# Kernel tuning notes

Hardware: AMD Instinct MI355X
Metric: run time of the kernel (lower is better)

The kernel has to match this reference:

```python
import jax, jax.numpy as jnp
import numpy as np

EPS = 1e-8

def unit_projection(x):
    # project each embedding vector so its Fourier coefficients have unit magnitude
    f = jnp.fft.fft(x, axis=-1)
    f = f / jnp.maximum(jnp.abs(f), EPS)
    return jnp.real(jnp.fft.ifft(f, axis=-1))

def bind(a, b):
    return jnp.fft.irfft(jnp.fft.rfft(a, axis=-1) * jnp.fft.rfft(b, axis=-1), n=a.shape[-1], axis=-1)

def unbind(s, k):
    # k is unit-magnitude in Fourier domain, so its inverse is its conjugate
    return jnp.fft.irfft(jnp.fft.rfft(s, axis=-1) * jnp.conj(jnp.fft.rfft(k, axis=-1)), n=s.shape[-1], axis=-1)

def layer_norm(x, g, b):
    mu = jnp.mean(x, axis=-1, keepdims=True)
    var = jnp.var(x, axis=-1, keepdims=True)
    return (x - mu) * jax.lax.rsqrt(var + 1e-5) * g + b

def setup_inputs():
    key = jax.random.key(0)
    ks = jax.random.split(key, 12)
    B, S, D = 4, 2048, 1024
    sc = 1.0 / np.sqrt(D)
    inp = {
        'x': jax.random.normal(ks[0], (B, S, D), jnp.float32),
        'Wq': jax.random.normal(ks[1], (D, D), jnp.float32) * sc,
        'bq': jnp.zeros((D,), jnp.float32),
        'Wk': jax.random.normal(ks[2], (D, D), jnp.float32) * sc,
        'bk': jnp.zeros((D,), jnp.float32),
        'Wv': jax.random.normal(ks[3], (D, D), jnp.float32) * sc,
        'bv': jnp.zeros((D,), jnp.float32),
        'ln1_g': jnp.ones((D,), jnp.float32), 'ln1_b': jnp.zeros((D,), jnp.float32),
        'ln2_g': jnp.ones((D,), jnp.float32), 'ln2_b': jnp.zeros((D,), jnp.float32),
        'W1': jax.random.normal(ks[4], (D, 4 * D), jnp.float32) * sc,
        'b1': jnp.zeros((4 * D,), jnp.float32),
        'W2': jax.random.normal(ks[5], (4 * D, D), jnp.float32) * (1.0 / np.sqrt(4 * D)),
        'b2': jnp.zeros((D,), jnp.float32),
    }
    return inp

def reference(x, Wq, bq, Wk, bk, Wv, bv, ln1_g, ln1_b, ln2_g, ln2_b, W1, b1, W2, b2):
    h = layer_norm(x, ln1_g, ln1_b)
    q = unit_projection(h @ Wq + bq)
    k = unit_projection(h @ Wk + bk)
    v = unit_projection(h @ Wv + bv)
    s = jnp.cumsum(bind(k, v), axis=1)  # causal prefix-sum over sequence
    mixed = unbind(s, q)
    x = x + mixed  # dropout=0.0
    h2 = layer_norm(x, ln2_g, ln2_b)
    mlp = jax.nn.gelu(h2 @ W1 + b1, approximate=False) @ W2 + b2
    return x + mlp
```

## Files before the change

### kernel.cpp

```cpp
#include <hip/hip_runtime.h>
#include <cstdint>
#include <cstddef>

#define DD 1024
#define SSEQ 2048
#define NB 4
#define MROWS 8192
#define FBINS 513
#define FPAD 520
#define WFP 1152
#define NQKV 3456
#define NHID 4096
#define NCHUNK 64
#define SCHUNK 32

typedef _Float16 f16_t;
typedef _Float16 f16x8 __attribute__((ext_vector_type(8)));
typedef _Float16 f16x2 __attribute__((ext_vector_type(2)));
typedef float f32x4 __attribute__((ext_vector_type(4)));

__device__ __forceinline__ float2 cmul(float2 a, float2 b) {
  return make_float2(a.x * b.x - a.y * b.y, a.x * b.y + a.y * b.x);
}

__device__ __forceinline__ void async_cp16(const void* g, void* l) {
  __builtin_amdgcn_global_load_lds(
      (const __attribute__((address_space(1))) void*)g,
      (__attribute__((address_space(3))) void*)l, 16, 0, 0);
}

__device__ __forceinline__ float fast_gelu(float val) {
  float av = __builtin_fabsf(val);
  float z = av * 0.70710678118654752f;
  float t = __builtin_amdgcn_rcpf(__builtin_fmaf(0.3275911f, z, 1.0f));
  float poly = t * __builtin_fmaf(t,
      __builtin_fmaf(t, __builtin_fmaf(t,
          __builtin_fmaf(t, 1.061405429f, -1.453152027f),
          1.421413741f), -0.284496736f), 0.254829592f);
  float e = __builtin_amdgcn_exp2f(z * z * -1.4426950408889634f);
  float w = poly * e;
  float r = fmaxf(val, 0.0f);
  return __builtin_fmaf(-0.5f * av, w, r);
}

__device__ __forceinline__ void fft1024(float2* bufA, float2* bufB,
                                        const float2* tw, int tid) {
  float2* s = bufA;
  float2* d = bufB;
  for (int m = 1; m < 1024; m <<= 1) {
#pragma unroll
    for (int r2 = 0; r2 < 2; ++r2) {
      int u = tid + r2 * 256;
      int k = u & (m - 1);
      int jm = u - k;
      float2 c0 = s[u];
      float2 c1 = s[u + 512];
      float2 wt = tw[jm];
      float2 su = make_float2(c0.x + c1.x, c0.y + c1.y);
      float2 df = make_float2(c0.x - c1.x, c0.y - c1.y);
      float2 pr = cmul(wt, df);
      d[2 * jm + k] = su;
      d[2 * jm + k + m] = pr;
    }
    __syncthreads();
    float2* tmp = s; s = d; d = tmp;
  }
}

__device__ __forceinline__ float2* fft512(float2* bufA, float2* bufB,
                                          const float2* tw, int tid) {
  float2* s = bufA;
  float2* d = bufB;
  for (int m = 1; m < 512; m <<= 1) {
    int u = tid;
    int k = u & (m - 1);
    int jm = u - k;
    float2 c0 = s[u];
    float2 c1 = s[u + 256];
    float2 wt = tw[jm];
    float2 su = make_float2(c0.x + c1.x, c0.y + c1.y);
    float2 df = make_float2(c0.x - c1.x, c0.y - c1.y);
    float2 pr = cmul(wt, df);
    d[2 * jm + k] = su;
    d[2 * jm + k + m] = pr;
    __syncthreads();
    float2* tmp = s; s = d; d = tmp;
  }
  return s;
}

__global__ __launch_bounds__(256) void wfft_k(
    const float* __restrict__ Wq, const float* __restrict__ Wk,
    const float* __restrict__ Wv, float* __restrict__ WfAll) {
  __shared__ float2 tw[512];
  __shared__ float2 bufA[1024];
  __shared__ float2 bufB[1024];
  const int tid = threadIdx.x;
  const int p = blockIdx.x >> 10, k = blockIdx.x & 1023;
  const float* W = (p == 0) ? Wq : ((p == 1) ? Wk : Wv);
  for (int t = tid; t < 512; t += 256) {
    float ang = -6.2831853071795864769f * (float)t * (1.0f / 1024.0f);
    tw[t] = make_float2(cosf(ang), sinf(ang));
  }
  const float* src = W + (size_t)k * DD;
  for (int t = tid; t < 1024; t += 256) bufA[t] = make_float2(src[t], 0.f);
  __syncthreads();
  fft1024(bufA, bufB, tw, tid);
  float* dst = WfAll + ((size_t)p * DD + k) * WFP;
  for (int t = tid; t <= 512; t += 256) {
    float2 f = bufA[t];
    dst[2 * t] = f.x;
    dst[2 * t + 1] = f.y;
  }
  for (int j = 1026 + tid; j < WFP; j += 256) dst[j] = 0.f;
}

__global__ __launch_bounds__(256) void bfft_k(
    const float* __restrict__ bq, const float* __restrict__ bk,
    const float* __restrict__ bv, float* __restrict__ biasC) {
  __shared__ float2 tw[512];
  __shared__ float2 bufA[1024];
  __shared__ float2 bufB[1024];
  const int tid = threadIdx.x;
  const int p = blockIdx.x;
  const float* bsrc = (p == 0) ? bq : ((p == 1) ? bk : bv);
  for (int t = tid; t < 512; t += 256) {
    float ang = -6.2831853071795864769f * (float)t * (1.0f / 1024.0f);
    tw[t] = make_float2(cosf(ang), sinf(ang));
  }
  for (int t = tid; t < 1024; t += 256) bufA[t] = make_float2(bsrc[t], 0.f);
  __syncthreads();
  fft1024(bufA, bufB, tw, tid);
  float* dst = biasC + (size_t)p * WFP;
  for (int t = tid; t <= 512; t += 256) {
    float2 f = bufA[t];
    dst[2 * t] = f.x;
    dst[2 * t + 1] = f.y;
  }
  for (int j = 1026 + tid; j < WFP; j += 256) dst[j] = 0.f;
}

__global__ __launch_bounds__(256) void transpose_cast_k(
    const float* __restrict__ W, f16_t* __restrict__ Wt, int K, int N) {
  __shared__ float tile[32][33];
  const int tx = threadIdx.x & 31, ty = threadIdx.x >> 5;
  const int n0 = blockIdx.x * 32, k0 = blockIdx.y * 32;
#pragma unroll
  for (int i = 0; i < 32; i += 8)
    tile[ty + i][tx] = W[(size_t)(k0 + ty + i) * N + n0 + tx];
  __syncthreads();
#pragma unroll
  for (int i = 0; i < 32; i += 8)
    Wt[(size_t)(n0 + ty + i) * K + k0 + tx] = (f16_t)tile[tx][ty + i];
}

__global__ __launch_bounds__(256) void transpose_cast2_k(
    const float* __restrict__ W, f16_t* __restrict__ WtH,
    f16_t* __restrict__ WtL, int K, int N) {
  __shared__ float tile[32][33];
  const int tx = threadIdx.x & 31, ty = threadIdx.x >> 5;
  const int n0 = blockIdx.x * 32, k0 = blockIdx.y * 32;
#pragma unroll
  for (int i = 0; i < 32; i += 8)
    tile[ty + i][tx] = W[(size_t)(k0 + ty + i) * N + n0 + tx];
  __syncthreads();
#pragma unroll
  for (int i = 0; i < 32; i += 8) {
    float val = tile[tx][ty + i];
    f16_t hi = (f16_t)val;
    f16_t lo = (f16_t)(val - (float)hi);
    size_t idx = (size_t)(n0 + ty + i) * K + k0 + tx;
    WtH[idx] = hi;
    WtL[idx] = lo;
  }
}

__global__ __launch_bounds__(256) void ln_cast2_k(
    const float* __restrict__ x, const float* __restrict__ g,
    const float* __restrict__ b, f16_t* __restrict__ hH,
    f16_t* __restrict__ hL) {
  const int row = blockIdx.x, tid = threadIdx.x;
  __shared__ float red[8];
  const float* xr = x + (size_t)row * DD;
  float v[4], ls = 0.f, lq = 0.f;
#pragma unroll
  for (int i = 0; i < 4; ++i) {
    v[i] = xr[i * 256 + tid];
    ls += v[i];
    lq += v[i] * v[i];
  }
#pragma unroll
  for (int o = 32; o > 0; o >>= 1) {
    ls += __shfl_down(ls, o);
    lq += __shfl_down(lq, o);
  }
  const int lane = tid & 63, w = tid >> 6;
  if (lane == 0) { red[w] = ls; red[w + 4] = lq; }
  __syncthreads();
  const float S = red[0] + red[1] + red[2] + red[3];
  const float Q = red[4] + red[5] + red[6] + red[7];
  const float mean = S * (1.f / 1024.f);
  const float var = Q * (1.f / 1024.f) - mean * mean;
  const float rs = rsqrtf(var + 1e-5f);
#pragma unroll
  for (int i = 0; i < 4; ++i) {
    int n = i * 256 + tid;
    float val = (v[i] - mean) * rs * g[n] + b[n];
    f16_t hi = (f16_t)val;
    hH[(size_t)row * DD + n] = hi;
    hL[(size_t)row * DD + n] = (f16_t)(val - (float)hi);
  }
}

__global__ __launch_bounds__(256, 2) void gemm_qkv_k(
    const f16_t* __restrict__ Ahi, const f16_t* __restrict__ Alo,
    const f16_t* __restrict__ Bhi, const float* __restrict__ bias,
    float* __restrict__ outF) {
  __shared__ alignas(16) f16_t AsH[128 * 64];
  __shared__ alignas(16) f16_t AsL[128 * 64];
  __shared__ alignas(16) f16_t BsH[128 * 64];
  const int tid = threadIdx.x;
  const int lane = tid & 63;
  const int w = tid >> 6;
  const int wm = w >> 1, wn = w & 1;

  const int lin = blockIdx.x;
  const int s = (lin & 7) * 216 + (lin >> 3);
  const int g = s / 108;
  const int r = s % 108;
  const int n = r >> 2;
  const int m0 = g * 4 + (r & 3);
  const int bn = n * 128;
  const int bm = m0 * 128;
  const bool qmode = (n < 9);

  f32x4 acc[4][4];
#pragma unroll
  for (int i = 0; i < 4; ++i)
#pragma unroll
    for (int j = 0; j < 4; ++j) acc[i][j] = (f32x4){0.f, 0.f, 0.f, 0.f};

  const int srow = lane >> 3;
  const int slot = lane & 7;

  for (int kt = 0; kt < 1024; kt += 64) {
#pragma unroll
    for (int i = 0; i < 4; ++i) {
      const int rb = (i * 4 + w) * 8;
      const int row = rb + srow;
      const int gg = (slot - (row & 7)) & 7;
      size_t ga = (size_t)(bm + row) * 1024 + kt + gg * 8;
      size_t gb = (size_t)(bn + row) * 1024 + kt + gg * 8;
      async_cp16(Ahi + ga, &AsH[rb * 64]);
      if (qmode) async_cp16(Alo + ga, &AsL[rb * 64]);
      async_cp16(Bhi + gb, &BsH[rb * 64]);
    }
    __syncthreads();
#pragma unroll
    for (int ks = 0; ks < 2; ++ks) {
      const int cgbase = ks * 4 + (lane >> 4);
      f16x8 ah[4], bh[4];
#pragma unroll
      for (int mt = 0; mt < 4; ++mt) {
        int m = wm * 64 + mt * 16 + (lane & 15);
        int sl = (cgbase + (m & 7)) & 7;
        ah[mt] = *(const f16x8*)(&AsH[m * 64 + sl * 8]);
      }
#pragma unroll
      for (int nt = 0; nt < 4; ++nt) {
        int nn = wn * 64 + nt * 16 + (lane & 15);
        int sl = (cgbase + (nn & 7)) & 7;
        bh[nt] = *(const f16x8*)(&BsH[nn * 64 + sl * 8]);
      }
#pragma unroll
      for (int mt = 0; mt < 4; ++mt)
#pragma unroll
        for (int nt = 0; nt < 4; ++nt)
          acc[mt][nt] = __builtin_amdgcn_mfma_f32_16x16x32_f16(
              ah[mt], bh[nt], acc[mt][nt], 0, 0, 0);
      if (qmode) {
        f16x8 al[4];
#pragma unroll
        for (int mt = 0; mt < 4; ++mt) {
          int m = wm * 64 + mt * 16 + (lane & 15);
          int sl = (cgbase + (m & 7)) & 7;
          al[mt] = *(const f16x8*)(&AsL[m * 64 + sl * 8]);
        }
#pragma unroll
        for (int mt = 0; mt < 4; ++mt)
#pragma unroll
          for (int nt = 0; nt < 4; ++nt)
            acc[mt][nt] = __builtin_amdgcn_mfma_f32_16x16x32_f16(
                al[mt], bh[nt], acc[mt][nt], 0, 0, 0);
      }
    }
    __syncthreads();
  }

  const int q = lane >> 4;
  const int cn = lane & 15;
#pragma unroll
  for (int mt = 0; mt < 4; ++mt) {
#pragma unroll
    for (int nt = 0; nt < 4; ++nt) {
      const int gcol = bn + wn * 64 + nt * 16 + cn;
      const float bv = bias[gcol];
      const int grow0 = bm + wm * 64 + mt * 16 + q * 4;
#pragma unroll
      for (int i = 0; i < 4; ++i) {
        size_t idx = (size_t)(grow0 + i) * NQKV + gcol;
        outF[idx] = acc[mt][nt][i] + bv;
      }
    }
  }
}

template <int EPI>
__global__ __launch_bounds__(256, 2) void gemm_bt_k(
    const f16_t* __restrict__ A, const f16_t* __restrict__ Bt,
    const float* __restrict__ bias, const float* __restrict__ resid,
    float* __restrict__ outF, f16_t* __restrict__ outH, int M, int N, int K) {
  __shared__ alignas(16) f16_t As[128 * 64];
  __shared__ alignas(16) f16_t Bs[128 * 64];
  const int tid = threadIdx.x;
  const int lane = tid & 63;
  const int w = tid >> 6;
  const int wm = w >> 1, wn = w & 1;
  int bm, bn;
  if (EPI == 2) {
    const int ntn = N >> 7;
    const int per = ((N >> 7) * (M >> 7)) >> 3;
    const int s = ((int)blockIdx.x & 7) * per + ((int)blockIdx.x >> 3);
    const int half = ntn * 2;
    const int g = s / half;
    const int r = s % half;
    bn = (r >> 1) * 128;
    bm = (g * 2 + (r & 1)) * 128;
  } else {
    bm = blockIdx.y * 128;
    bn = blockIdx.x * 128;
  }

  f32x4 acc[4][4];
#pragma unroll
  for (int i = 0; i < 4; ++i)
#pragma unroll
    for (int j = 0; j < 4; ++j) acc[i][j] = (f32x4){0.f, 0.f, 0.f, 0.f};

  const int srow = lane >> 3;
  const int slot = lane & 7;

  for (int kt = 0; kt < K; kt += 64) {
#pragma unroll
    for (int i = 0; i < 4; ++i) {
      const int rb = (i * 4 + w) * 8;
      const int row = rb + srow;
      const int gg = (slot - (row & 7)) & 7;
      const f16_t* ga = A + (size_t)(bm + row) * K + kt + gg * 8;
      const f16_t* gb = Bt + (size_t)(bn + row) * K + kt + gg * 8;
      async_cp16(ga, &As[rb * 64]);
      async_cp16(gb, &Bs[rb * 64]);
    }
    __syncthreads();
#pragma unroll
    for (int ks = 0; ks < 2; ++ks) {
      const int cgbase = ks * 4 + (lane >> 4);
      f16x8 af[4], bfv[4];
#pragma unroll
      for (int mt = 0; mt < 4; ++mt) {
        int m = wm * 64 + mt * 16 + (lane & 15);
        int sl = (cgbase + (m & 7)) & 7;
        af[mt] = *(const f16x8*)(&As[m * 64 + sl * 8]);
      }
#pragma unroll
      for (int nt = 0; nt < 4; ++nt) {
        int nn = wn * 64 + nt * 16 + (lane & 15);
        int sl = (cgbase + (nn & 7)) & 7;
        bfv[nt] = *(const f16x8*)(&Bs[nn * 64 + sl * 8]);
      }
#pragma unroll
      for (int mt = 0; mt < 4; ++mt)
#pragma unroll
        for (int nt = 0; nt < 4; ++nt)
          acc[mt][nt] = __builtin_amdgcn_mfma_f32_16x16x32_f16(
              af[mt], bfv[nt], acc[mt][nt], 0, 0, 0);
    }
    __syncthreads();
  }

  const int q = lane >> 4;
  const int cn = lane & 15;
#pragma unroll
  for (int mt = 0; mt < 4; ++mt) {
#pragma unroll
    for (int nt = 0; nt < 4; ++nt) {
      const int gcol = bn + wn * 64 + nt * 16 + cn;
      const float bv = bias[gcol];
      const int grow0 = bm + wm * 64 + mt * 16 + q * 4;
#pragma unroll
      for (int i = 0; i < 4; ++i) {
        float val = acc[mt][nt][i] + bv;
        size_t idx = (size_t)(grow0 + i) * N + gcol;
        if (EPI == 1) {
          outH[idx] = (f16_t)fast_gelu(val);
        } else {
          outF[idx] = val + resid[idx];
        }
      }
    }
  }
}

__device__ __forceinline__ float2 unitc(float2 a) {
  float inv = 1.0f / fmaxf(sqrtf(a.x * a.x + a.y * a.y), 1e-8f);
  return make_float2(a.x * inv, a.y * inv);
}
__device__ __forceinline__ float2 bind_bin(const float2* r, int f) {
  float2 kn = unitc(r[576 + f]);
  float2 vn = unitc(r[1152 + f]);
  return cmul(kn, vn);
}

__global__ __launch_bounds__(256) void scan_pass1_k(
    const float* __restrict__ qkvF, float2* __restrict__ T) {
  const int bid = blockIdx.x;
  const int sc = bid & 63;
  const int fh = (bid >> 6) & 1;
  const int b = bid >> 7;
  const int s0 = sc * SCHUNK;
  const float2* base = (const float2*)(qkvF + ((size_t)(b * SSEQ + s0)) * NQKV);
  for (int f = fh * 256 + threadIdx.x; f < FBINS; f += 512) {
    float2 acc = make_float2(0.f, 0.f);
    const float2* r = base;
    for (int i = 0; i < SCHUNK; ++i) {
      float2 pv = bind_bin(r, f);
      acc.x += pv.x; acc.y += pv.y;
      r += NQKV / 2;
    }
    T[((size_t)b * NCHUNK + sc) * FBINS + f] = acc;
  }
}

__global__ void scan_pass2_k(float2* __restrict__ T) {
  const int idx = blockIdx.x * 256 + threadIdx.x;
  if (idx >= NB * FBINS) return;
  const int b = idx / FBINS, f = idx % FBINS;
  float2 acc = make_float2(0.f, 0.f);
  for (int sc = 0; sc < NCHUNK; ++sc) {
    size_t a = ((size_t)b * NCHUNK + sc) * FBINS + f;
    float2 v = T[a];
    T[a] = acc;
    acc.x += v.x; acc.y += v.y;
  }
}

__global__ __launch_bounds__(256) void scan_pass3_k(
    const float* __restrict__ qkvF, const float2* __restrict__ T,
    float2* __restrict__ Scum) {
  const int bid = blockIdx.x;
  const int sc = bid & 63;
  const int fh = (bid >> 6) & 1;
  const int b = bid >> 7;
  const int s0 = sc * SCHUNK;
  const float2* base = (const float2*)(qkvF + ((size_t)(b * SSEQ + s0)) * NQKV);
  for (int f = fh * 256 + threadIdx.x; f < FBINS; f += 512) {
    float2 acc = T[((size_t)b * NCHUNK + sc) * FBINS + f];
    const float2* r = base;
    size_t orow = ((size_t)(b * SSEQ + s0)) * FPAD + f;
    for (int i = 0; i < SCHUNK; ++i) {
      float2 pv = bind_bin(r, f);
      acc.x += pv.x; acc.y += pv.y;
      Scum[orow] = acc;
      r += NQKV / 2;
      orow += FPAD;
    }
  }
}

__global__ __launch_bounds__(256) void unbind_ln2_k(
    const float2* __restrict__ Scum, const float* __restrict__ qkvF,
    const float* __restrict__ x, float* __restrict__ x2out,
    f16_t* __restrict__ h2, const float* __restrict__ g2,
    const float* __restrict__ b2) {
  __shared__ float2 tw[256];
  __shared__ float2 Marr[513];
  __shared__ float2 bufA[512];
  __shared__ float2 bufB[512];
  __shared__ float red[8];
  const int tid = threadIdx.x;
  const int row = blockIdx.x;

  {
    float ang = 6.2831853071795864769f * (float)tid * (1.0f / 512.0f);
    tw[tid] = make_float2(cosf(ang), sinf(ang));
  }
  const float2* qrow = (const float2*)(qkvF + (size_t)row * NQKV);
  for (int t = tid; t <= 512; t += 256) {
    float2 sc = Scum[(size_t)row * FPAD + t];
    float2 fq = unitc(qrow[t]);
    Marr[t] = make_float2(sc.x * fq.x + sc.y * fq.y, sc.y * fq.x - sc.x * fq.y);
  }
  __syncthreads();
#pragma unroll
  for (int rr = 0; rr < 2; ++rr) {
    int t = tid + rr * 256;
    float2 a = Marr[t];
    float2 b = Marr[512 - t];
    float2 E = make_float2(0.5f * (a.x + b.x), 0.5f * (a.y - b.y));
    float2 Dd = make_float2(0.5f * (a.x - b.x), 0.5f * (a.y + b.y));
    float ang = 6.2831853071795864769f * (float)t * (1.0f / 1024.0f);
    float cw = cosf(ang), sw = sinf(ang);
    float2 O = make_float2(cw * Dd.x - sw * Dd.y, cw * Dd.y + sw * Dd.x);
    bufA[t] = make_float2(E.x - O.y, E.y + O.x);
  }
  __syncthreads();
  float2* res = fft512(bufA, bufB, tw, tid);

  const float* xr = x + (size_t)row * DD;
  float v[2][2];
  float ls = 0.f, lq = 0.f;
#pragma unroll
  for (int rr = 0; rr < 2; ++rr) {
    int n = tid + rr * 256;
    float2 z = res[n];
    float2 xv = *(const float2*)(xr + 2 * n);
    float v0 = xv.x + z.x * (1.0f / 512.0f);
    float v1 = xv.y + z.y * (1.0f / 512.0f);
    *(float2*)(x2out + (size_t)row * DD + 2 * n) = make_float2(v0, v1);
    v[rr][0] = v0; v[rr][1] = v1;
    ls += v0 + v1;
    lq += v0 * v0 + v1 * v1;
  }
#pragma unroll
  for (int o = 32; o > 0; o >>= 1) {
    ls += __shfl_down(ls, o);
    lq += __shfl_down(lq, o);
  }
  const int lane = tid & 63, w = tid >> 6;
  if (lane == 0) { red[w] = ls; red[w + 4] = lq; }
  __syncthreads();
  const float S = red[0] + red[1] + red[2] + red[3];
  const float Q = red[4] + red[5] + red[6] + red[7];
  const float mean = S * (1.f / 1024.f);
  const float var = Q * (1.f / 1024.f) - mean * mean;
  const float rs = rsqrtf(var + 1e-5f);
  f16_t* hr = h2 + (size_t)row * DD;
#pragma unroll
  for (int rr = 0; rr < 2; ++rr) {
    int n = tid + rr * 256;
    float2 gv = *(const float2*)(g2 + 2 * n);
    float2 bv = *(const float2*)(b2 + 2 * n);
    f16x2 hp;
    hp[0] = (f16_t)((v[rr][0] - mean) * rs * gv.x + bv.x);
    hp[1] = (f16_t)((v[rr][1] - mean) * rs * gv.y + bv.y);
    *(f16x2*)(hr + 2 * n) = hp;
  }
}

extern "C" void kernel_launch(void* const* d_in, const int* in_sizes, int n_in,
                              void* d_out, int out_size, void* d_ws,
                              size_t ws_size, hipStream_t stream) {
  const float* x     = (const float*)d_in[0];
  const float* Wq    = (const float*)d_in[1];
  const float* bq    = (const float*)d_in[2];
  const float* Wk    = (const float*)d_in[3];
  const float* bk    = (const float*)d_in[4];
  const float* Wv    = (const float*)d_in[5];
  const float* bv    = (const float*)d_in[6];
  const float* ln1_g = (const float*)d_in[7];
  const float* ln1_b = (const float*)d_in[8];
  const float* ln2_g = (const float*)d_in[9];
  const float* ln2_b = (const float*)d_in[10];
  const float* W1    = (const float*)d_in[11];
  const float* b1    = (const float*)d_in[12];
  const float* W2    = (const float*)d_in[13];
  const float* b2    = (const float*)d_in[14];
  float* out = (float*)d_out;

  char* p = (char*)d_ws;
  auto take = [&](size_t bytes) {
    char* r = p;
    p += (bytes + 255) & ~(size_t)255;
    return r;
  };
  f16_t* BtH   = (f16_t*)take((size_t)NQKV * DD * sizeof(f16_t));
  f16_t* BtL   = (f16_t*)take((size_t)NQKV * DD * sizeof(f16_t));
  f16_t* W1T   = (f16_t*)take((size_t)NHID * DD * sizeof(f16_t));
  f16_t* W2T   = (f16_t*)take((size_t)DD * NHID * sizeof(f16_t));
  float* biasC = (float*)take((size_t)NQKV * sizeof(float));
  f16_t* hbuf  = (f16_t*)take((size_t)MROWS * DD * sizeof(f16_t));
  char*  big   = take((size_t)MROWS * NQKV * sizeof(float));
  float2* Scum = (float2*)take((size_t)MROWS * FPAD * sizeof(float2));
  float* x2    = (float*)take((size_t)MROWS * DD * sizeof(float));
  float2* Tch  = (float2*)take((size_t)NB * NCHUNK * FBINS * sizeof(float2));
  float* WfAll   = (float*)big;
  float* qkv_f   = (float*)big;
  f16_t* mlp1    = (f16_t*)big;
  f16_t* hlo     = (f16_t*)x2;

  wfft_k<<<3 * DD, 256, 0, stream>>>(Wq, Wk, Wv, WfAll);
  for (int pp = 0; pp < 3; ++pp)
    transpose_cast2_k<<<dim3(WFP / 32, DD / 32), 256, 0, stream>>>(
        WfAll + (size_t)pp * DD * WFP,
        BtH + (size_t)pp * WFP * DD,
        BtL + (size_t)pp * WFP * DD, DD, WFP);
  bfft_k<<<3, 256, 0, stream>>>(bq, bk, bv, biasC);
  transpose_cast_k<<<dim3(128, 32), 256, 0, stream>>>(W1, W1T, DD, NHID);
  transpose_cast_k<<<dim3(32, 128), 256, 0, stream>>>(W2, W2T, NHID, DD);

  ln_cast2_k<<<MROWS, 256, 0, stream>>>(x, ln1_g, ln1_b, hbuf, hlo);

  gemm_qkv_k<<<(NQKV / 128) * (MROWS / 128), 256, 0, stream>>>(
      hbuf, hlo, BtH, biasC, qkv_f);

  scan_pass1_k<<<NB * NCHUNK * 2, 256, 0, stream>>>(qkv_f, Tch);
  scan_pass2_k<<<(NB * FBINS + 255) / 256, 256, 0, stream>>>(Tch);
  scan_pass3_k<<<NB * NCHUNK * 2, 256, 0, stream>>>(qkv_f, Tch, Scum);

  unbind_ln2_k<<<MROWS, 256, 0, stream>>>(Scum, qkv_f, x, x2, hbuf, ln2_g, ln2_b);

  gemm_bt_k<1><<<dim3(NHID / 128, MROWS / 128), 256, 0, stream>>>(
      hbuf, W1T, b1, nullptr, nullptr, mlp1, MROWS, NHID, DD);

  gemm_bt_k<2><<<(DD / 128) * (MROWS / 128), 256, 0, stream>>>(
      mlp1, W2T, b2, x2, out, nullptr, MROWS, DD, NHID);
}
```

Baseline: 533.3 us.

## Replace MLP GEMMs with 8-wave double-buffered ping-pong pipelined kernel

Replaces the 128x128 single-buffered MLP GEMM with a 512-thread kernel using larger 256x256 / 128x256 tiles and double-buffered LDS. Global-to-LDS async copies for the next K-tile are issued in quarters, interleaved with MFMA quarters, and gated by explicit vmcnt waits, barriers and setprio. Block indices are remapped so that consecutive blocks are spread across the eight XCDs. This is meant to hide global load latency and increase data reuse. In exchange it raises register and LDS pressure and relies on hand-counted waitcnt values being correct.

```diff
diff --git a/kernel.cpp b/kernel.cpp
--- a/kernel.cpp
+++ b/kernel.cpp
@@ -28,6 +28,13 @@
       (const __attribute__((address_space(1))) void*)g,
       (__attribute__((address_space(3))) void*)l, 16, 0, 0);
 }
+
+template <int N> __device__ __forceinline__ void vwait();
+template <> __device__ __forceinline__ void vwait<0>() { asm volatile("s_waitcnt vmcnt(0)" ::: "memory"); }
+template <> __device__ __forceinline__ void vwait<1>() { asm volatile("s_waitcnt vmcnt(1)" ::: "memory"); }
+template <> __device__ __forceinline__ void vwait<2>() { asm volatile("s_waitcnt vmcnt(2)" ::: "memory"); }
+template <> __device__ __forceinline__ void vwait<3>() { asm volatile("s_waitcnt vmcnt(3)" ::: "memory"); }
+template <> __device__ __forceinline__ void vwait<4>() { asm volatile("s_waitcnt vmcnt(4)" ::: "memory"); }
 
 __device__ __forceinline__ float fast_gelu(float val) {
   float av = __builtin_fabsf(val);
@@ -315,100 +322,186 @@
   }
 }
 
-template <int EPI>
-__global__ __launch_bounds__(256, 2) void gemm_bt_k(
+template <int RHALF>
+__device__ __forceinline__ void stage_half(const f16_t* __restrict__ G,
+                                           int grow0, int ldk, int kt,
+                                           f16_t* ls, int w, int lane) {
+  const int srow = lane >> 3;
+  const int slot = lane & 7;
+#pragma unroll
+  for (int j = 0; j < RHALF / 64; ++j) {
+    const int rb = (w + j * 8) * 8;
+    const int row = rb + srow;
+    const int gg = (slot - (row & 7)) & 7;
+    async_cp16(G + (size_t)(grow0 + row) * ldk + kt + gg * 8, ls + rb * 64);
+  }
+}
+
+template <int BM, int BN>
+__device__ __forceinline__ void readA(const f16_t* As, int mq, int wm, int lane,
+                                      f16x8 (&aR)[BM / 64][2]) {
+#pragma unroll
+  for (int mf = 0; mf < BM / 64; ++mf) {
+    const int m = mq * (BM / 2) + wm * (BM / 4) + mf * 16 + (lane & 15);
+#pragma unroll
+    for (int ks = 0; ks < 2; ++ks) {
+      const int cg = ks * 4 + (lane >> 4);
+      const int sl = (cg + (m & 7)) & 7;
+      aR[mf][ks] = *(const f16x8*)(As + m * 64 + sl * 8);
+    }
+  }
+}
+
+template <int BM, int BN>
+__device__ __forceinline__ void readB(const f16_t* Bs, int nq, int wn, int lane,
+                                      f16x8 (&bR)[BN / 128][2]) {
+#pragma unroll
+  for (int nf = 0; nf < BN / 128; ++nf) {
+    const int n = nq * (BN / 2) + wn * (BN / 8) + nf * 16 + (lane & 15);
+#pragma unroll
+    for (int ks = 0; ks < 2; ++ks) {
+      const int cg = ks * 4 + (lane >> 4);
+      const int sl = (cg + (n & 7)) & 7;
+      bR[nf][ks] = *(const f16x8*)(Bs + n * 64 + sl * 8);
+    }
+  }
+}
+
+template <int MF, int NF>
+__device__ __forceinline__ void mfma_q(f32x4 (&acc)[MF][NF],
+                                       const f16x8 (&aR)[MF][2],
+                                       const f16x8 (&bR)[NF][2]) {
+#pragma unroll
+  for (int ks = 0; ks < 2; ++ks)
+#pragma unroll
+    for (int mf = 0; mf < MF; ++mf)
+#pragma unroll
+      for (int nf = 0; nf < NF; ++nf)
+        acc[mf][nf] = __builtin_amdgcn_mfma_f32_16x16x32_f16(
+            aR[mf][ks], bR[nf][ks], acc[mf][nf], 0, 0, 0);
+}
+
+template <int BM, int BN, int MM, int NN, int KK, int EPI>
+__global__ __launch_bounds__(512, 2) void gemm8p_k(
     const f16_t* __restrict__ A, const f16_t* __restrict__ Bt,
     const float* __restrict__ bias, const float* __restrict__ resid,
-    float* __restrict__ outF, f16_t* __restrict__ outH, int M, int N, int K) {
-  __shared__ alignas(16) f16_t As[128 * 64];
-  __shared__ alignas(16) f16_t Bs[128 * 64];
+    float* __restrict__ outF, f16_t* __restrict__ outH) {
+  constexpr int MF = BM / 64;
+  constexpr int NF = BN / 128;
+  constexpr int LA = BM / 128;
+  constexpr int LB = BN / 128;
+  constexpr int NT = KK / 64;
+  constexpr int TILE = (BM + BN) * 64;
+  __shared__ alignas(16) f16_t lds[2 * TILE];
+
   const int tid = threadIdx.x;
   const int lane = tid & 63;
   const int w = tid >> 6;
-  const int wm = w >> 1, wn = w & 1;
-  int bm, bn;
-  if (EPI == 2) {
-    const int ntn = N >> 7;
-    const int per = ((N >> 7) * (M >> 7)) >> 3;
-    const int s = ((int)blockIdx.x & 7) * per + ((int)blockIdx.x >> 3);
-    const int half = ntn * 2;
-    const int g = s / half;
-    const int r = s % half;
-    bn = (r >> 1) * 128;
-    bm = (g * 2 + (r & 1)) * 128;
-  } else {
-    bm = blockIdx.y * 128;
-    bn = blockIdx.x * 128;
-  }
-
-  f32x4 acc[4][4];
-#pragma unroll
-  for (int i = 0; i < 4; ++i)
-#pragma unroll
-    for (int j = 0; j < 4; ++j) acc[i][j] = (f32x4){0.f, 0.f, 0.f, 0.f};
-
-  const int srow = lane >> 3;
-  const int slot = lane & 7;
-
-  for (int kt = 0; kt < K; kt += 64) {
-#pragma unroll
-    for (int i = 0; i < 4; ++i) {
-      const int rb = (i * 4 + w) * 8;
-      const int row = rb + srow;
-      const int gg = (slot - (row & 7)) & 7;
-      const f16_t* ga = A + (size_t)(bm + row) * K + kt + gg * 8;
-      const f16_t* gb = Bt + (size_t)(bn + row) * K + kt + gg * 8;
-      async_cp16(ga, &As[rb * 64]);
-      async_cp16(gb, &Bs[rb * 64]);
-    }
-    __syncthreads();
-#pragma unroll
-    for (int ks = 0; ks < 2; ++ks) {
-      const int cgbase = ks * 4 + (lane >> 4);
-      f16x8 af[4], bfv[4];
-#pragma unroll
-      for (int mt = 0; mt < 4; ++mt) {
-        int m = wm * 64 + mt * 16 + (lane & 15);
-        int sl = (cgbase + (m & 7)) & 7;
-        af[mt] = *(const f16x8*)(&As[m * 64 + sl * 8]);
-      }
-#pragma unroll
-      for (int nt = 0; nt < 4; ++nt) {
-        int nn = wn * 64 + nt * 16 + (lane & 15);
-        int sl = (cgbase + (nn & 7)) & 7;
-        bfv[nt] = *(const f16x8*)(&Bs[nn * 64 + sl * 8]);
-      }
-#pragma unroll
-      for (int mt = 0; mt < 4; ++mt)
-#pragma unroll
-        for (int nt = 0; nt < 4; ++nt)
-          acc[mt][nt] = __builtin_amdgcn_mfma_f32_16x16x32_f16(
-              af[mt], bfv[nt], acc[mt][nt], 0, 0, 0);
-    }
-    __syncthreads();
-  }
-
-  const int q = lane >> 4;
+  const int wm = w >> 2;
+  const int wn = w & 3;
+
+  constexpr int ntm = MM / BM, ntn = NN / BN;
+  constexpr int per = (ntm * ntn) / 8;
+  const int lin = (int)blockIdx.x;
+  const int s = (lin & 7) * per + (lin >> 3);
+  const int bn = (s % ntn) * BN;
+  const int bm = (s / ntn) * BM;
+
+  f32x4 acc[2][2][MF][NF];
+#pragma unroll
+  for (int a0 = 0; a0 < 2; ++a0)
+#pragma unroll
+    for (int a1 = 0; a1 < 2; ++a1)
+#pragma unroll
+      for (int mf = 0; mf < MF; ++mf)
+#pragma unroll
+        for (int nf = 0; nf < NF; ++nf)
+          acc[a0][a1][mf][nf] = (f32x4){0.f, 0.f, 0.f, 0.f};
+
+  {
+    f16_t* A0s = lds;
+    f16_t* B0s = lds + BM * 64;
+    stage_half<BM / 2>(A, bm, KK, 0, A0s, w, lane);
+    stage_half<BN / 2>(Bt, bn, KK, 0, B0s, w, lane);
+    stage_half<BN / 2>(Bt, bn + BN / 2, KK, 0, B0s + (BN / 2) * 64, w, lane);
+    stage_half<BM / 2>(A, bm + BM / 2, KK, 0, A0s + (BM / 2) * 64, w, lane);
+  }
+  vwait<LA + LB>();
+  __builtin_amdgcn_s_barrier();
+
+  f16x8 aR[MF][2], bR0[NF][2], bR1[NF][2];
+
+  for (int t = 0; t < NT; ++t) {
+    const int cur = t & 1;
+    f16_t* As = lds + cur * TILE;
+    f16_t* Bs = As + BM * 64;
+    f16_t* Asn = lds + (cur ^ 1) * TILE;
+    f16_t* Bsn = Asn + BM * 64;
+    const bool pre = (t + 1 < NT);
+    const int ktn = (t + 1) << 6;
+
+    readA<BM, BN>(As, 0, wm, lane, aR);
+    readB<BM, BN>(Bs, 0, wn, lane, bR0);
+    if (pre) stage_half<BM / 2>(A, bm, KK, ktn, Asn, w, lane);
+    __builtin_amdgcn_s_barrier();
+    __builtin_amdgcn_s_setprio(1);
+    mfma_q<MF, NF>(acc[0][0], aR, bR0);
+    __builtin_amdgcn_s_setprio(0);
+    if (pre) vwait<2 * LA>(); else vwait<LA>();
+    __builtin_amdgcn_s_barrier();
+
+    readB<BM, BN>(Bs, 1, wn, lane, bR1);
+    if (pre) stage_half<BN / 2>(Bt, bn, KK, ktn, Bsn, w, lane);
+    __builtin_amdgcn_s_barrier();
+    __builtin_amdgcn_s_setprio(1);
+    mfma_q<MF, NF>(acc[0][1], aR, bR1);
+    __builtin_amdgcn_s_setprio(0);
+    if (pre) vwait<LA + LB>(); else vwait<0>();
+    __builtin_amdgcn_s_barrier();
+
+    readA<BM, BN>(As, 1, wm, lane, aR);
+    if (pre) stage_half<BN / 2>(Bt, bn + BN / 2, KK, ktn,
+                                Bsn + (BN / 2) * 64, w, lane);
+    __builtin_amdgcn_s_barrier();
+    __builtin_amdgcn_s_setprio(1);
+    mfma_q<MF, NF>(acc[1][0], aR, bR0);
+    __builtin_amdgcn_s_setprio(0);
+    __builtin_amdgcn_s_barrier();
+
+    if (pre) stage_half<BM / 2>(A, bm + BM / 2, KK, ktn,
+                                Asn + (BM / 2) * 64, w, lane);
+    __builtin_amdgcn_s_barrier();
+    __builtin_amdgcn_s_setprio(1);
+    mfma_q<MF, NF>(acc[1][1], aR, bR1);
+    __builtin_amdgcn_s_setprio(0);
+    if (pre) vwait<LA + LB>();
+    __builtin_amdgcn_s_barrier();
+  }
+
+  const int q4 = lane >> 4;
   const int cn = lane & 15;
 #pragma unroll
-  for (int mt = 0; mt < 4; ++mt) {
-#pragma unroll
-    for (int nt = 0; nt < 4; ++nt) {
-      const int gcol = bn + wn * 64 + nt * 16 + cn;
-      const float bv = bias[gcol];
-      const int grow0 = bm + wm * 64 + mt * 16 + q * 4;
-#pragma unroll
-      for (int i = 0; i < 4; ++i) {
-        float val = acc[mt][nt][i] + bv;
-        size_t idx = (size_t)(grow0 + i) * N + gcol;
-        if (EPI == 1) {
-          outH[idx] = (f16_t)fast_gelu(val);
-        } else {
-          outF[idx] = val + resid[idx];
+  for (int mq = 0; mq < 2; ++mq)
+#pragma unroll
+    for (int nq = 0; nq < 2; ++nq)
+#pragma unroll
+      for (int mf = 0; mf < MF; ++mf)
+#pragma unroll
+        for (int nf = 0; nf < NF; ++nf) {
+          const int gcol = bn + nq * (BN / 2) + wn * (BN / 8) + nf * 16 + cn;
+          const float bv = bias[gcol];
+          const int grow0 = bm + mq * (BM / 2) + wm * (BM / 4) + mf * 16 + q4 * 4;
+#pragma unroll
+          for (int i = 0; i < 4; ++i) {
+            const float val = acc[mq][nq][mf][nf][i] + bv;
+            const size_t idx = (size_t)(grow0 + i) * NN + gcol;
+            if (EPI == 1) {
+              outH[idx] = (f16_t)fast_gelu(val);
+            } else {
+              outF[idx] = val + resid[idx];
+            }
+          }
         }
-      }
-    }
-  }
 }
 
 __device__ __forceinline__ float2 unitc(float2 a) {
@@ -619,9 +712,9 @@
 
   unbind_ln2_k<<<MROWS, 256, 0, stream>>>(Scum, qkv_f, x, x2, hbuf, ln2_g, ln2_b);
 
-  gemm_bt_k<1><<<dim3(NHID / 128, MROWS / 128), 256, 0, stream>>>(
-      hbuf, W1T, b1, nullptr, nullptr, mlp1, MROWS, NHID, DD);
-
-  gemm_bt_k<2><<<(DD / 128) * (MROWS / 128), 256, 0, stream>>>(
-      mlp1, W2T, b2, x2, out, nullptr, MROWS, DD, NHID);
-}
+  gemm8p_k<256, 256, MROWS, NHID, DD, 1><<<512, 512, 0, stream>>>(
+      hbuf, W1T, b1, nullptr, nullptr, mlp1);
+
+  gemm8p_k<128, 256, MROWS, DD, NHID, 2><<<256, 512, 0, stream>>>(
+      mlp1, W2T, b2, x2, out, nullptr);
+}
```

Measured after the change: 497.0 us. 6.8% less time.
